# Kernel optimization log

Hardware: AMD Instinct MI355X
Metric: run time of the kernel (lower is better)

Reference implementation:

```python
import jax, jax.numpy as jnp
import numpy as np

D = 1024      # d_model
H = 8         # heads
DH = D // H
L = 12        # layers
E = 4         # experts
F = 2048      # dim_feedforward
NCLS = 10
SPARSITY = 0.5
EPS = 1e-5
B, S = 4, 512


def _xavier(key, shape):
    fan_in, fan_out = shape[-1], shape[-2] if len(shape) > 1 else shape[-1]
    scale = jnp.sqrt(2.0 / (fan_in + fan_out))
    return jax.random.normal(key, shape, jnp.float32) * scale


def setup_inputs() -> dict:
    key = jax.random.key(0)
    ks = jax.random.split(key, 16)
    return {
        "x": jax.random.normal(ks[0], (B, S, D), jnp.float32),
        "pos": jax.random.normal(ks[1], (1, 512, D), jnp.float32) * 0.02,
        # stacked per-layer transformer params
        "Wqkv": _xavier(ks[2], (L, 3 * D, D)), "bqkv": jnp.zeros((L, 3 * D), jnp.float32),
        "Wo": _xavier(ks[3], (L, D, D)),       "bo": jnp.zeros((L, D), jnp.float32),
        "ln1_s": jnp.ones((L, D), jnp.float32), "ln1_b": jnp.zeros((L, D), jnp.float32),
        "W1": _xavier(ks[4], (L, F, D)), "b1": jnp.zeros((L, F), jnp.float32),
        "W2": _xavier(ks[5], (L, D, F)), "b2": jnp.zeros((L, D), jnp.float32),
        "ln2_s": jnp.ones((L, D), jnp.float32), "ln2_b": jnp.zeros((L, D), jnp.float32),
        # shared gate / experts / classifier
        "Wg": _xavier(ks[6], (E, D)), "bg": jnp.zeros((E,), jnp.float32),
        "We": _xavier(ks[7], (E, D, D)), "be": jnp.zeros((E, D), jnp.float32),
        "Wf": _xavier(ks[8], (NCLS, D)), "bf": jnp.zeros((NCLS,), jnp.float32),
    }


def _layernorm(x, s, b):
    m = jnp.mean(x, axis=-1, keepdims=True)
    v = jnp.mean(jnp.square(x - m), axis=-1, keepdims=True)
    return (x - m) * jax.lax.rsqrt(v + EPS) * s + b


def _forward(x, pos, Wqkv, bqkv, Wo, bo, ln1_s, ln1_b, W1, b1, W2, b2,
             ln2_s, ln2_b, Wg, bg, We, be, Wf, bf):
    Bx, Sx, _ = x.shape
    x = x + pos[:, :Sx, :]
    for l in range(L):
        # --- self-attention (post-norm TransformerEncoderLayer, eval/no-dropout) ---
        qkv = x @ Wqkv[l].T + bqkv[l]                      # [B,S,3D]
        q, k, v = jnp.split(qkv, 3, axis=-1)
        q = q.reshape(Bx, Sx, H, DH).transpose(0, 2, 1, 3)  # bhsd
        k = k.reshape(Bx, Sx, H, DH).transpose(0, 2, 1, 3)
        v = v.reshape(Bx, Sx, H, DH).transpose(0, 2, 1, 3)
        attn = jax.nn.softmax(jnp.einsum('bhqd,bhkd->bhqk', q, k) / jnp.sqrt(jnp.float32(DH)), axis=-1)
        o = jnp.einsum('bhqk,bhkd->bhqd', attn, v).transpose(0, 2, 1, 3).reshape(Bx, Sx, D)
        o = o @ Wo[l].T + bo[l]
        x = _layernorm(x + o, ln1_s[l], ln1_b[l])
        # --- ffn (exact gelu) ---
        h = jax.nn.gelu(x @ W1[l].T + b1[l], approximate=False) @ W2[l].T + b2[l]
        x = _layernorm(x + h, ln2_s[l], ln2_b[l])
        # --- top-2 gated MoE (shared gate/experts across layers) ---
        gs = jax.nn.softmax(x @ Wg.T + bg, axis=-1)         # [B,S,E]
        vals, idx = jax.lax.top_k(gs, 2)                    # [B,S,2]
        all_out = jnp.einsum('bsd,eod->bseo', x, We) + be   # [B,S,E,D]
        sel = jnp.take_along_axis(all_out, idx[..., None], axis=2)  # [B,S,2,D]
        expert_out = jnp.sum(sel * vals[..., None], axis=2)
        x = x * (1.0 - SPARSITY) + expert_out * SPARSITY
    return x[:, -1, :] @ Wf.T + bf                          # [B,10]


def reference(x, pos, Wqkv, bqkv, Wo, bo, ln1_s, ln1_b, W1, b1, W2, b2,
              ln2_s, ln2_b, Wg, bg, We, be, Wf, bf):
    return _forward(x, pos, Wqkv, bqkv, Wo, bo, ln1_s, ln1_b, W1, b1, W2, b2,
                    ln2_s, ln2_b, Wg, bg, We, be, Wf, bf)
```

## Files before the change

### kernel.cpp

```cpp
#include <hip/hip_runtime.h>
#include <math.h>

#define D     1024
#define NH    8
#define DHD   128
#define NL    12
#define NE    4
#define FF    2048
#define NCLS  10
#define BB    4
#define SS    512
#define TT    (BB*SS)
#define EPSV  1e-5f
#define SPARS 0.5f

typedef __attribute__((ext_vector_type(8))) short bf16x8;
typedef __attribute__((ext_vector_type(4))) float f32x4;
typedef unsigned short ushortT;

__device__ __forceinline__ ushortT f2bf(float f) {
    unsigned u = __float_as_uint(f);
    u += 0x7FFF + ((u >> 16) & 1);
    return (ushortT)(u >> 16);
}
__device__ __forceinline__ float bf2f(ushortT h) {
    return __uint_as_float(((unsigned)h) << 16);
}

__global__ __launch_bounds__(256)
void wconv(const float* __restrict__ in, ushortT* __restrict__ out, long n)
{
    const long stride = (long)gridDim.x * 256 * 8;
    for (long i = ((long)blockIdx.x * 256 + threadIdx.x) * 8; i < n; i += stride) {
        float f[8];
        *reinterpret_cast<float4*>(f)   = *reinterpret_cast<const float4*>(in + i);
        *reinterpret_cast<float4*>(f+4) = *reinterpret_cast<const float4*>(in + i + 4);
        bf16x8 u;
        #pragma unroll
        for (int e = 0; e < 8; ++e) ((ushortT*)&u)[e] = f2bf(f[e]);
        *reinterpret_cast<bf16x8*>(out + i) = u;
    }
}

#define LDP 40

template<int MODE, int SK, int ACT, int BN>
__global__ __launch_bounds__(256)
void gemm_mfma(const ushortT* __restrict__ A, const ushortT* __restrict__ Bw,
               const float* __restrict__ bias, void* __restrict__ Cv,
               int M, int N, int Ktot, int Klen, long eBw, long eBias, long eC)
{
    const int z = blockIdx.z;
    int koff = 0;
    float* Cf = nullptr; ushortT* Ch = nullptr;
    if constexpr (SK > 1) {
        koff = z * Klen;
        Cf = (float*)Cv + (size_t)z * M * N;
    } else {
        Bw   += (size_t)z * eBw;
        bias += (size_t)z * eBias;
        if constexpr (MODE == 0) Ch = (ushortT*)Cv + (size_t)z * eC;
        else                     Cf = (float*)Cv   + (size_t)z * eC;
    }

    constexpr int MR = (BN == 128) ? 4 : 2;
    __shared__ ushortT Asl[128 * LDP];
    __shared__ ushortT Bsl[BN * LDP];

    const int tid  = threadIdx.x;
    const int wave = tid >> 6, lane = tid & 63;
    const int wm = (BN == 128) ? (wave >> 1) * 64 : wave * 32;
    const int wn = (BN == 128) ? (wave & 1) * 64 : 0;
    const int fr = lane & 15;
    const int fq = lane >> 4;

    const int m0 = blockIdx.y * 128;
    const int n0 = blockIdx.x * BN;

    const int arow = tid >> 1;
    const int akc  = (tid & 1) * 16;
    const ushortT* Ag = A + (size_t)(m0 + arow) * Ktot + koff + akc;
    const int brow = (BN == 128) ? (tid >> 1) : (tid >> 2);
    const int bkc  = (BN == 128) ? (tid & 1) * 16 : (tid & 3) * 8;
    const ushortT* Bg = Bw + (size_t)(n0 + brow) * Ktot + koff + bkc;

    f32x4 acc[MR][4] = {};

    for (int k0 = 0; k0 < Klen; k0 += 32) {
        bf16x8 av8[2], bv8[2];
        av8[0] = *reinterpret_cast<const bf16x8*>(Ag + k0);
        av8[1] = *reinterpret_cast<const bf16x8*>(Ag + k0 + 8);
        bv8[0] = *reinterpret_cast<const bf16x8*>(Bg + k0);
        if constexpr (BN == 128)
            bv8[1] = *reinterpret_cast<const bf16x8*>(Bg + k0 + 8);
        __syncthreads();
        *reinterpret_cast<bf16x8*>(&Asl[arow*LDP + akc])     = av8[0];
        *reinterpret_cast<bf16x8*>(&Asl[arow*LDP + akc + 8]) = av8[1];
        *reinterpret_cast<bf16x8*>(&Bsl[brow*LDP + bkc])     = bv8[0];
        if constexpr (BN == 128)
            *reinterpret_cast<bf16x8*>(&Bsl[brow*LDP + bkc + 8]) = bv8[1];
        __syncthreads();

        bf16x8 af[MR], bfr[4];
        #pragma unroll
        for (int i = 0; i < MR; ++i)
            af[i]  = *reinterpret_cast<const bf16x8*>(&Asl[(wm + i*16 + fr)*LDP + fq*8]);
        #pragma unroll
        for (int j = 0; j < 4; ++j)
            bfr[j] = *reinterpret_cast<const bf16x8*>(&Bsl[(wn + j*16 + fr)*LDP + fq*8]);
        #pragma unroll
        for (int i = 0; i < MR; ++i)
            #pragma unroll
            for (int j = 0; j < 4; ++j)
                acc[i][j] = __builtin_amdgcn_mfma_f32_16x16x32_bf16(af[i], bfr[j], acc[i][j], 0, 0, 0);
    }

    #pragma unroll
    for (int j = 0; j < 4; ++j) {
        const int n = n0 + wn + j*16 + fr;
        float bb = 0.f;
        if constexpr (SK == 1) bb = bias[n];
        #pragma unroll
        for (int i = 0; i < MR; ++i) {
            const int mb = m0 + wm + i*16 + fq*4;
            if constexpr (SK > 1) {
                #pragma unroll
                for (int r = 0; r < 4; ++r)
                    Cf[(size_t)(mb + r) * N + n] = acc[i][j][r];
            } else if constexpr (MODE == 0) {
                #pragma unroll
                for (int r = 0; r < 4; ++r) {
                    float u = acc[i][j][r] + bb;
                    if constexpr (ACT == 1) u = 0.5f*u*(1.0f + erff(u*0.70710678118654752f));
                    Ch[(size_t)(mb + r) * N + n] = f2bf(u);
                }
            } else {
                #pragma unroll
                for (int r = 0; r < 4; ++r) {
                    float u = acc[i][j][r] + bb;
                    if constexpr (ACT == 1) u = 0.5f*u*(1.0f + erff(u*0.70710678118654752f));
                    Cf[(size_t)(mb + r) * N + n] = u;
                }
            }
        }
    }
}

__global__ __launch_bounds__(256)
void kv_prep(const float* __restrict__ qkv, ushortT* __restrict__ Kb, ushortT* __restrict__ Vt)
{
    __shared__ ushortT T[64*136];
    const int tid = threadIdx.x;
    const int st = blockIdx.x, bh = blockIdx.y;
    const int b = bh >> 3, h = bh & 7;
    const float* base = qkv + (size_t)(b*SS + st*64)*3*D + h*DHD;

    #pragma unroll
    for (int p = 0; p < 4; ++p) {
        const int row = (tid >> 4) + 16*p;
        const int colb = (tid & 15) * 8;
        {
            const float* src = base + (size_t)row*3*D + D + colb;
            float f[8];
            *reinterpret_cast<float4*>(f)   = *reinterpret_cast<const float4*>(src);
            *reinterpret_cast<float4*>(f+4) = *reinterpret_cast<const float4*>(src+4);
            bf16x8 u;
            #pragma unroll
            for (int e = 0; e < 8; ++e) ((ushortT*)&u)[e] = f2bf(f[e]);
            *reinterpret_cast<bf16x8*>(&Kb[((size_t)bh*SS + st*64 + row)*DHD + colb]) = u;
        }
        {
            const float* src = base + (size_t)row*3*D + 2*D + colb;
            float f[8];
            *reinterpret_cast<float4*>(f)   = *reinterpret_cast<const float4*>(src);
            *reinterpret_cast<float4*>(f+4) = *reinterpret_cast<const float4*>(src+4);
            #pragma unroll
            for (int e = 0; e < 8; ++e) T[row*136 + colb + e] = f2bf(f[e]);
        }
    }
    __syncthreads();
    #pragma unroll
    for (int p = 0; p < 4; ++p) {
        const int d  = (tid >> 3) + 32*p;
        const int sb = (tid & 7) * 8;
        bf16x8 u;
        #pragma unroll
        for (int e = 0; e < 8; ++e) ((ushortT*)&u)[e] = T[(sb + e)*136 + d];
        *reinterpret_cast<bf16x8*>(&Vt[((size_t)bh*DHD + d)*SS + st*64 + sb]) = u;
    }
}

#define KLP 136
#define VLP 72
#define PLP 72

__global__ __launch_bounds__(256)
void attn_mfma(const float* __restrict__ qkv, const ushortT* __restrict__ Kb,
               const ushortT* __restrict__ Vt, ushortT* __restrict__ o16)
{
    __shared__ ushortT Kl[64*KLP];
    __shared__ ushortT Vl[128*VLP];
    __shared__ ushortT Pl[4*16*PLP];

    const int tid = threadIdx.x;
    const int w = tid >> 6, lane = tid & 63;
    const int g = lane >> 4, c = lane & 15;
    const int bh = blockIdx.y;
    const int b = bh >> 3, h = bh & 7;
    const int q0 = blockIdx.x*64 + w*16;
    ushortT* Pw = Pl + w*16*PLP;

    bf16x8 qhi[4], qlo[4];
    const float scale = 0.08838834764831845f;
    {
        const float* Qrow = qkv + (size_t)(b*SS + q0 + c)*3*D + h*DHD;
        #pragma unroll
        for (int db = 0; db < 4; ++db) {
            float f[8];
            *reinterpret_cast<float4*>(f)   = *reinterpret_cast<const float4*>(Qrow + db*32 + g*8);
            *reinterpret_cast<float4*>(f+4) = *reinterpret_cast<const float4*>(Qrow + db*32 + g*8 + 4);
            #pragma unroll
            for (int e = 0; e < 8; ++e) {
                const float fs = f[e]*scale;
                const ushortT hi = f2bf(fs);
                ((ushortT*)&qhi[db])[e] = hi;
                ((ushortT*)&qlo[db])[e] = f2bf(fs - bf2f(hi));
            }
        }
    }

    const ushortT* Kg = Kb + (size_t)bh*SS*DHD;
    const ushortT* Vg = Vt + (size_t)bh*DHD*SS;

    float m_r[4], l_r[4];
    #pragma unroll
    for (int r = 0; r < 4; ++r) { m_r[r] = -1e30f; l_r[r] = 0.f; }
    f32x4 oacc[8] = {};

    for (int kt = 0; kt < SS/64; ++kt) {
        __syncthreads();
        #pragma unroll
        for (int p = 0; p < 4; ++p) {
            const int row = (tid >> 4) + 16*p;
            const int colb = (tid & 15)*8;
            bf16x8 u = *reinterpret_cast<const bf16x8*>(&Kg[(size_t)(kt*64 + row)*DHD + colb]);
            *reinterpret_cast<bf16x8*>(&Kl[row*KLP + colb]) = u;
        }
        #pragma unroll
        for (int p = 0; p < 4; ++p) {
            const int dr = (tid >> 3) + 32*p;
            const int sb = (tid & 7)*8;
            bf16x8 u = *reinterpret_cast<const bf16x8*>(&Vg[(size_t)dr*SS + kt*64 + sb]);
            *reinterpret_cast<bf16x8*>(&Vl[dr*VLP + sb]) = u;
        }
        __syncthreads();

        f32x4 s[4] = {};
        #pragma unroll
        for (int db = 0; db < 4; ++db) {
            bf16x8 kf[4];
            #pragma unroll
            for (int kb = 0; kb < 4; ++kb)
                kf[kb] = *reinterpret_cast<const bf16x8*>(&Kl[(kb*16 + c)*KLP + db*32 + g*8]);
            #pragma unroll
            for (int kb = 0; kb < 4; ++kb) {
                s[kb] = __builtin_amdgcn_mfma_f32_16x16x32_bf16(qhi[db], kf[kb], s[kb], 0, 0, 0);
                s[kb] = __builtin_amdgcn_mfma_f32_16x16x32_bf16(qlo[db], kf[kb], s[kb], 0, 0, 0);
            }
        }

        float tmax[4];
        #pragma unroll
        for (int r = 0; r < 4; ++r)
            tmax[r] = fmaxf(fmaxf(s[0][r], s[1][r]), fmaxf(s[2][r], s[3][r]));
        #pragma unroll
        for (int off = 1; off < 16; off <<= 1)
            #pragma unroll
            for (int r = 0; r < 4; ++r)
                tmax[r] = fmaxf(tmax[r], __shfl_xor(tmax[r], off));
        float mn[4], corr[4];
        #pragma unroll
        for (int r = 0; r < 4; ++r) {
            mn[r] = fmaxf(m_r[r], tmax[r]);
            corr[r] = __expf(m_r[r] - mn[r]);
            m_r[r] = mn[r];
        }
        float tsum[4] = {0.f, 0.f, 0.f, 0.f};
        #pragma unroll
        for (int kb = 0; kb < 4; ++kb)
            #pragma unroll
            for (int r = 0; r < 4; ++r) {
                const float p = __expf(s[kb][r] - mn[r]);
                s[kb][r] = p;
                tsum[r] += p;
            }
        #pragma unroll
        for (int off = 1; off < 16; off <<= 1)
            #pragma unroll
            for (int r = 0; r < 4; ++r)
                tsum[r] += __shfl_xor(tsum[r], off);
        #pragma unroll
        for (int r = 0; r < 4; ++r) l_r[r] = l_r[r]*corr[r] + tsum[r];
        #pragma unroll
        for (int df = 0; df < 8; ++df)
            #pragma unroll
            for (int r = 0; r < 4; ++r)
                oacc[df][r] *= corr[r];

        #pragma unroll
        for (int kb = 0; kb < 4; ++kb)
            #pragma unroll
            for (int r = 0; r < 4; ++r)
                Pw[(g*4 + r)*PLP + kb*16 + c] = f2bf(s[kb][r]);

        #pragma unroll
        for (int kk = 0; kk < 2; ++kk) {
            bf16x8 pa = *reinterpret_cast<const bf16x8*>(&Pw[c*PLP + kk*32 + g*8]);
            #pragma unroll
            for (int df = 0; df < 8; ++df) {
                bf16x8 vb = *reinterpret_cast<const bf16x8*>(&Vl[(df*16 + c)*VLP + kk*32 + g*8]);
                oacc[df] = __builtin_amdgcn_mfma_f32_16x16x32_bf16(pa, vb, oacc[df], 0, 0, 0);
            }
        }
    }

    #pragma unroll
    for (int r = 0; r < 4; ++r) {
        const float inv = 1.0f / l_r[r];
        ushortT* orow = o16 + (size_t)(b*SS + q0 + g*4 + r)*D + h*DHD + c;
        #pragma unroll
        for (int df = 0; df < 8; ++df)
            orow[df*16] = f2bf(oacc[df][r] * inv);
    }
}

template<int SK, int GATE>
__global__ __launch_bounds__(256)
void add_ln_r(const float* __restrict__ xin, const float* __restrict__ P,
              const float* __restrict__ dbias,
              const float* __restrict__ gs, const float* __restrict__ gb,
              float* __restrict__ x32, ushortT* __restrict__ x16,
              const float* __restrict__ Wg, const float* __restrict__ bg,
              float* __restrict__ gv, int* __restrict__ gi)
{
    const int row = blockIdx.x, tid = threadIdx.x;
    const size_t off = (size_t)row*D + tid*4;
    float4 a = *reinterpret_cast<const float4*>(xin + off);
    float d0, d1, d2, d3;
    {
        float4 bvd = *reinterpret_cast<const float4*>(dbias + tid*4);
        d0 = bvd.x; d1 = bvd.y; d2 = bvd.z; d3 = bvd.w;
    }
    #pragma unroll
    for (int s = 0; s < SK; ++s) {
        float4 pv = *reinterpret_cast<const float4*>(P + (size_t)s*TT*D + off);
        d0 += pv.x; d1 += pv.y; d2 += pv.z; d3 += pv.w;
    }
    float v0=a.x+d0, v1=a.y+d1, v2=a.z+d2, v3=a.w+d3;
    __shared__ float red[2][4];
    float s = v0+v1+v2+v3;
    #pragma unroll
    for (int o = 32; o; o >>= 1) s += __shfl_xor(s, o, 64);
    if ((tid & 63) == 0) red[0][tid>>6] = s;
    __syncthreads();
    const float mean = (red[0][0]+red[0][1]+red[0][2]+red[0][3]) * (1.0f/D);
    v0-=mean; v1-=mean; v2-=mean; v3-=mean;
    float qv = v0*v0+v1*v1+v2*v2+v3*v3;
    #pragma unroll
    for (int o = 32; o; o >>= 1) qv += __shfl_xor(qv, o, 64);
    if ((tid & 63) == 0) red[1][tid>>6] = qv;
    __syncthreads();
    const float var = (red[1][0]+red[1][1]+red[1][2]+red[1][3]) * (1.0f/D);
    const float rstd = rsqrtf(var + EPSV);
    float4 sv = *reinterpret_cast<const float4*>(gs + tid*4);
    float4 bv = *reinterpret_cast<const float4*>(gb + tid*4);
    float ov[4];
    ov[0] = v0*rstd*sv.x + bv.x;
    ov[1] = v1*rstd*sv.y + bv.y;
    ov[2] = v2*rstd*sv.z + bv.z;
    ov[3] = v3*rstd*sv.w + bv.w;
    float4 o4; o4.x=ov[0]; o4.y=ov[1]; o4.z=ov[2]; o4.w=ov[3];
    *reinterpret_cast<float4*>(x32 + off) = o4;
    ushort4 h4; h4.x=f2bf(ov[0]); h4.y=f2bf(ov[1]); h4.z=f2bf(ov[2]); h4.w=f2bf(ov[3]);
    *reinterpret_cast<ushort4*>(x16 + off) = h4;

    if constexpr (GATE) {
        float p[4] = {0.f, 0.f, 0.f, 0.f};
        #pragma unroll
        for (int e = 0; e < 4; ++e) {
            const float* wr = Wg + (size_t)e*D + tid*4;
            p[e] = ov[0]*wr[0] + ov[1]*wr[1] + ov[2]*wr[2] + ov[3]*wr[3];
        }
        #pragma unroll
        for (int o = 32; o; o >>= 1) {
            p[0] += __shfl_xor(p[0], o, 64); p[1] += __shfl_xor(p[1], o, 64);
            p[2] += __shfl_xor(p[2], o, 64); p[3] += __shfl_xor(p[3], o, 64);
        }
        __shared__ float gred[4][4];
        if ((tid & 63) == 0) {
            const int w = tid>>6;
            gred[w][0]=p[0]; gred[w][1]=p[1]; gred[w][2]=p[2]; gred[w][3]=p[3];
        }
        __syncthreads();
        if (tid == 0) {
            float g[4];
            #pragma unroll
            for (int e = 0; e < 4; ++e) g[e] = gred[0][e]+gred[1][e]+gred[2][e]+gred[3][e] + bg[e];
            const float mx = fmaxf(fmaxf(g[0],g[1]), fmaxf(g[2],g[3]));
            float ssum = 0.f;
            #pragma unroll
            for (int e = 0; e < 4; ++e) { g[e] = __expf(g[e]-mx); ssum += g[e]; }
            const float inv = 1.0f/ssum;
            #pragma unroll
            for (int e = 0; e < 4; ++e) g[e] *= inv;
            int i0 = 0;
            for (int e = 1; e < 4; ++e) if (g[e] > g[i0]) i0 = e;
            int i1 = (i0 == 0) ? 1 : 0;
            for (int e = 0; e < 4; ++e) if (e != i0 && g[e] > g[i1]) i1 = e;
            gv[row*2]   = g[i0]; gv[row*2+1] = g[i1];
            gi[row*2]   = i0;    gi[row*2+1] = i1;
        }
    }
}

__global__ __launch_bounds__(256)
void moe_combine(float* __restrict__ x, ushortT* __restrict__ x16,
                 const float* __restrict__ eo,
                 const float* __restrict__ gv, const int* __restrict__ gi)
{
    const size_t i = (size_t)blockIdx.x*256 + threadIdx.x;
    const int t = (int)(i >> 10);
    const float w0 = gv[t*2]*SPARS, w1 = gv[t*2+1]*SPARS;
    const size_t TD = (size_t)TT*D;
    const float e0 = eo[(size_t)gi[t*2]*TD + i];
    const float e1 = eo[(size_t)gi[t*2+1]*TD + i];
    const float r = x[i]*(1.0f-SPARS) + w0*e0 + w1*e1;
    x[i] = r;
    x16[i] = f2bf(r);
}

__global__ __launch_bounds__(256)
void addpos(const float* __restrict__ xin, const float* __restrict__ pos,
            float* __restrict__ xo, ushortT* __restrict__ x16)
{
    const size_t i = (size_t)blockIdx.x*256 + threadIdx.x;
    const float r = xin[i] + pos[i & ((size_t)SS*D - 1)];
    xo[i] = r;
    x16[i] = f2bf(r);
}

__global__ __launch_bounds__(64)
void final_kernel(const float* __restrict__ x, const float* __restrict__ Wf,
                  const float* __restrict__ bf, float* __restrict__ out)
{
    const int b = blockIdx.x / NCLS, n = blockIdx.x % NCLS;
    const float* xr = x + ((size_t)b*SS + SS-1)*D;
    const int tid = threadIdx.x;
    float s = 0.f;
    for (int d = tid; d < D; d += 64) s += xr[d]*Wf[(size_t)n*D + d];
    #pragma unroll
    for (int o = 32; o; o >>= 1) s += __shfl_xor(s, o, 64);
    if (tid == 0) out[b*NCLS + n] = s + bf[n];
}

extern "C" void kernel_launch(void* const* d_in, const int* in_sizes, int n_in,
                              void* d_out, int out_size, void* d_ws, size_t ws_size,
                              hipStream_t stream)
{
    const float* x_in = (const float*)d_in[0];
    const float* pos  = (const float*)d_in[1];
    const float* Wqkv = (const float*)d_in[2];
    const float* bqkv = (const float*)d_in[3];
    const float* Wo   = (const float*)d_in[4];
    const float* bo   = (const float*)d_in[5];
    const float* ln1s = (const float*)d_in[6];
    const float* ln1b = (const float*)d_in[7];
    const float* W1   = (const float*)d_in[8];
    const float* b1   = (const float*)d_in[9];
    const float* W2   = (const float*)d_in[10];
    const float* b2   = (const float*)d_in[11];
    const float* ln2s = (const float*)d_in[12];
    const float* ln2b = (const float*)d_in[13];
    const float* Wg   = (const float*)d_in[14];
    const float* bg   = (const float*)d_in[15];
    const float* We   = (const float*)d_in[16];
    const float* be   = (const float*)d_in[17];
    const float* Wf   = (const float*)d_in[18];
    const float* bf   = (const float*)d_in[19];
    float* out = (float*)d_out;

    const long nWqkv = (long)NL*3*D*D;
    const long nWo   = (long)NL*D*D;
    const long nW1   = (long)NL*FF*D;
    const long nW2   = (long)NL*D*FF;
    const long nWe   = (long)NE*D*D;

    float* ws     = (float*)d_ws;
    float*   xbuf  = ws;
    ushortT* xb16  = (ushortT*)(xbuf + (size_t)TT*D);
    ushortT* ob16  = xb16 + (size_t)TT*D;
    float*   scratch = (float*)(ob16 + (size_t)TT*D);
    ushortT* hb16 = (ushortT*)(scratch + (size_t)TT*D*4);
    float*   gv    = (float*)(hb16 + (size_t)TT*FF);
    int*     gi    = (int*)(gv + (size_t)TT*2);
    ushortT* wq16  = (ushortT*)(gi + (size_t)TT*2);
    ushortT* wo16  = wq16 + nWqkv;
    ushortT* w116  = wo16 + nWo;
    ushortT* w216  = w116 + nW1;
    ushortT* we16  = w216 + nW2;
    float*   qkvbuf = scratch;
    ushortT* Kb     = (ushortT*)(qkvbuf + (size_t)TT*3*D);
    ushortT* Vt     = Kb + (size_t)BB*NH*SS*DHD;
    float*   parts  = scratch;
    float*   ebuf   = scratch;

    const dim3 blk(256);
    wconv<<<dim3(2048), blk, 0, stream>>>(Wqkv, wq16, nWqkv);
    wconv<<<dim3(1024), blk, 0, stream>>>(Wo,   wo16, nWo);
    wconv<<<dim3(2048), blk, 0, stream>>>(W1,   w116, nW1);
    wconv<<<dim3(2048), blk, 0, stream>>>(W2,   w216, nW2);
    wconv<<<dim3(512),  blk, 0, stream>>>(We,   we16, nWe);

    addpos<<<dim3(TT*D/256), blk, 0, stream>>>(x_in, pos, xbuf, xb16);

    for (int l = 0; l < NL; ++l) {
        gemm_mfma<1,1,0,64><<<dim3(3*D/64, TT/128, 1), blk, 0, stream>>>(
            xb16, wq16 + (size_t)l*3*D*D, bqkv + (size_t)l*3*D, qkvbuf,
            TT, 3*D, D, D, 0, 0, 0);
        kv_prep<<<dim3(SS/64, BB*NH), blk, 0, stream>>>(qkvbuf, Kb, Vt);
        attn_mfma<<<dim3(SS/64, BB*NH), blk, 0, stream>>>(qkvbuf, Kb, Vt, ob16);
        gemm_mfma<1,4,0,128><<<dim3(D/128, TT/128, 4), blk, 0, stream>>>(
            ob16, wo16 + (size_t)l*D*D, bo, parts, TT, D, D, D/4, 0, 0, 0);
        add_ln_r<4,0><<<dim3(TT), blk, 0, stream>>>(
            xbuf, parts, bo + (size_t)l*D, ln1s + (size_t)l*D, ln1b + (size_t)l*D,
            xbuf, xb16, nullptr, nullptr, nullptr, nullptr);
        gemm_mfma<0,1,1,64><<<dim3(FF/64, TT/128, 1), blk, 0, stream>>>(
            xb16, w116 + (size_t)l*FF*D, b1 + (size_t)l*FF, hb16, TT, FF, D, D, 0, 0, 0);
        gemm_mfma<1,4,0,128><<<dim3(D/128, TT/128, 4), blk, 0, stream>>>(
            hb16, w216 + (size_t)l*D*FF, b2, parts, TT, D, FF, FF/4, 0, 0, 0);
        add_ln_r<4,1><<<dim3(TT), blk, 0, stream>>>(
            xbuf, parts, b2 + (size_t)l*D, ln2s + (size_t)l*D, ln2b + (size_t)l*D,
            xbuf, xb16, Wg, bg, gv, gi);
        gemm_mfma<1,1,0,64><<<dim3(D/64, TT/128, NE), blk, 0, stream>>>(
            xb16, we16, be, ebuf, TT, D, D, D, (long)D*D, (long)D, (long)TT*D);
        moe_combine<<<dim3(TT*D/256), blk, 0, stream>>>(xbuf, xb16, ebuf, gv, gi);
    }
    final_kernel<<<dim3(BB*NCLS), dim3(64), 0, stream>>>(xbuf, Wf, bf, out);
}
```

Measured before the change: 2.591 ms.

## Fuse QKV split/convert into GEMM epilogue and prefetch next K tile

The QKV GEMM epilogue now writes Q as fp32 in a compact layout, K directly as bf16 in head-major layout, and V as bf16, so the old kv_prep pass only has to transpose bf16 V. This removes the full fp32 qkv round trip for K and V. Separately, the GEMM main loop now loads the next K-slice from global memory into registers before the MFMA work on the current slice, overlapping load latency with compute at the cost of extra registers. The epilogue stores for K are scattered at 2-byte granularity, which may reduce write efficiency.

```diff
diff --git a/kernel.cpp b/kernel.cpp
--- a/kernel.cpp
+++ b/kernel.cpp
@@ -44,11 +44,12 @@
 
 #define LDP 40
 
-template<int MODE, int SK, int ACT, int BN>
+template<int MODE, int SK, int ACT, int BN, int EPI>
 __global__ __launch_bounds__(256)
 void gemm_mfma(const ushortT* __restrict__ A, const ushortT* __restrict__ Bw,
                const float* __restrict__ bias, void* __restrict__ Cv,
-               int M, int N, int Ktot, int Klen, long eBw, long eBias, long eC)
+               int M, int N, int Ktot, int Klen, long eBw, long eBias, long eC,
+               float* __restrict__ qp, ushortT* __restrict__ kp, ushortT* __restrict__ vp)
 {
     const int z = blockIdx.z;
     int koff = 0;
@@ -85,14 +86,15 @@
     const ushortT* Bg = Bw + (size_t)(n0 + brow) * Ktot + koff + bkc;
 
     f32x4 acc[MR][4] = {};
+    bf16x8 av8[2], bv8[2];
+
+    av8[0] = *reinterpret_cast<const bf16x8*>(Ag);
+    av8[1] = *reinterpret_cast<const bf16x8*>(Ag + 8);
+    bv8[0] = *reinterpret_cast<const bf16x8*>(Bg);
+    if constexpr (BN == 128)
+        bv8[1] = *reinterpret_cast<const bf16x8*>(Bg + 8);
 
     for (int k0 = 0; k0 < Klen; k0 += 32) {
-        bf16x8 av8[2], bv8[2];
-        av8[0] = *reinterpret_cast<const bf16x8*>(Ag + k0);
-        av8[1] = *reinterpret_cast<const bf16x8*>(Ag + k0 + 8);
-        bv8[0] = *reinterpret_cast<const bf16x8*>(Bg + k0);
-        if constexpr (BN == 128)
-            bv8[1] = *reinterpret_cast<const bf16x8*>(Bg + k0 + 8);
         __syncthreads();
         *reinterpret_cast<bf16x8*>(&Asl[arow*LDP + akc])     = av8[0];
         *reinterpret_cast<bf16x8*>(&Asl[arow*LDP + akc + 8]) = av8[1];
@@ -101,6 +103,15 @@
             *reinterpret_cast<bf16x8*>(&Bsl[brow*LDP + bkc + 8]) = bv8[1];
         __syncthreads();
 
+        const int kn = k0 + 32;
+        if (kn < Klen) {
+            av8[0] = *reinterpret_cast<const bf16x8*>(Ag + kn);
+            av8[1] = *reinterpret_cast<const bf16x8*>(Ag + kn + 8);
+            bv8[0] = *reinterpret_cast<const bf16x8*>(Bg + kn);
+            if constexpr (BN == 128)
+                bv8[1] = *reinterpret_cast<const bf16x8*>(Bg + kn + 8);
+        }
+
         bf16x8 af[MR], bfr[4];
         #pragma unroll
         for (int i = 0; i < MR; ++i)
@@ -123,7 +134,23 @@
         #pragma unroll
         for (int i = 0; i < MR; ++i) {
             const int mb = m0 + wm + i*16 + fq*4;
-            if constexpr (SK > 1) {
+            if constexpr (EPI == 1) {
+                #pragma unroll
+                for (int r = 0; r < 4; ++r) {
+                    const float u = acc[i][j][r] + bb;
+                    const int t = mb + r;
+                    if (n0 < D) {
+                        qp[(size_t)t*D + n] = u;
+                    } else if (n0 < 2*D) {
+                        const int n2 = n - D;
+                        const int hh = n2 >> 7, dd = n2 & 127;
+                        const int bb_ = t >> 9, ss_ = t & 511;
+                        kp[(((size_t)bb_*NH + hh)*SS + ss_)*DHD + dd] = f2bf(u);
+                    } else {
+                        vp[(size_t)t*D + (n - 2*D)] = f2bf(u);
+                    }
+                }
+            } else if constexpr (SK > 1) {
                 #pragma unroll
                 for (int r = 0; r < 4; ++r)
                     Cf[(size_t)(mb + r) * N + n] = acc[i][j][r];
@@ -147,36 +174,20 @@
 }
 
 __global__ __launch_bounds__(256)
-void kv_prep(const float* __restrict__ qkv, ushortT* __restrict__ Kb, ushortT* __restrict__ Vt)
+void v_tr(const ushortT* __restrict__ Vb, ushortT* __restrict__ Vt)
 {
     __shared__ ushortT T[64*136];
     const int tid = threadIdx.x;
     const int st = blockIdx.x, bh = blockIdx.y;
     const int b = bh >> 3, h = bh & 7;
-    const float* base = qkv + (size_t)(b*SS + st*64)*3*D + h*DHD;
+    const ushortT* base = Vb + (size_t)(b*SS + st*64)*D + h*DHD;
 
     #pragma unroll
     for (int p = 0; p < 4; ++p) {
         const int row = (tid >> 4) + 16*p;
         const int colb = (tid & 15) * 8;
-        {
-            const float* src = base + (size_t)row*3*D + D + colb;
-            float f[8];
-            *reinterpret_cast<float4*>(f)   = *reinterpret_cast<const float4*>(src);
-            *reinterpret_cast<float4*>(f+4) = *reinterpret_cast<const float4*>(src+4);
-            bf16x8 u;
-            #pragma unroll
-            for (int e = 0; e < 8; ++e) ((ushortT*)&u)[e] = f2bf(f[e]);
-            *reinterpret_cast<bf16x8*>(&Kb[((size_t)bh*SS + st*64 + row)*DHD + colb]) = u;
-        }
-        {
-            const float* src = base + (size_t)row*3*D + 2*D + colb;
-            float f[8];
-            *reinterpret_cast<float4*>(f)   = *reinterpret_cast<const float4*>(src);
-            *reinterpret_cast<float4*>(f+4) = *reinterpret_cast<const float4*>(src+4);
-            #pragma unroll
-            for (int e = 0; e < 8; ++e) T[row*136 + colb + e] = f2bf(f[e]);
-        }
+        bf16x8 u = *reinterpret_cast<const bf16x8*>(base + (size_t)row*D + colb);
+        *reinterpret_cast<bf16x8*>(&T[row*136 + colb]) = u;
     }
     __syncthreads();
     #pragma unroll
@@ -195,7 +206,7 @@
 #define PLP 72
 
 __global__ __launch_bounds__(256)
-void attn_mfma(const float* __restrict__ qkv, const ushortT* __restrict__ Kb,
+void attn_mfma(const float* __restrict__ Qb, const ushortT* __restrict__ Kb,
                const ushortT* __restrict__ Vt, ushortT* __restrict__ o16)
 {
     __shared__ ushortT Kl[64*KLP];
@@ -213,7 +224,7 @@
     bf16x8 qhi[4], qlo[4];
     const float scale = 0.08838834764831845f;
     {
-        const float* Qrow = qkv + (size_t)(b*SS + q0 + c)*3*D + h*DHD;
+        const float* Qrow = Qb + (size_t)(b*SS + q0 + c)*D + h*DHD;
         #pragma unroll
         for (int db = 0; db < 4; ++db) {
             float f[8];
@@ -508,9 +519,10 @@
     ushortT* w116  = wo16 + nWo;
     ushortT* w216  = w116 + nW1;
     ushortT* we16  = w216 + nW2;
-    float*   qkvbuf = scratch;
-    ushortT* Kb     = (ushortT*)(qkvbuf + (size_t)TT*3*D);
-    ushortT* Vt     = Kb + (size_t)BB*NH*SS*DHD;
+    float*   Qbuf = scratch;
+    ushortT* Kb   = (ushortT*)(Qbuf + (size_t)TT*D);
+    ushortT* Vb   = Kb + (size_t)TT*D;
+    ushortT* Vt   = Vb + (size_t)TT*D;
     float*   parts  = scratch;
     float*   ebuf   = scratch;
 
@@ -524,25 +536,29 @@
     addpos<<<dim3(TT*D/256), blk, 0, stream>>>(x_in, pos, xbuf, xb16);
 
     for (int l = 0; l < NL; ++l) {
-        gemm_mfma<1,1,0,64><<<dim3(3*D/64, TT/128, 1), blk, 0, stream>>>(
-            xb16, wq16 + (size_t)l*3*D*D, bqkv + (size_t)l*3*D, qkvbuf,
-            TT, 3*D, D, D, 0, 0, 0);
-        kv_prep<<<dim3(SS/64, BB*NH), blk, 0, stream>>>(qkvbuf, Kb, Vt);
-        attn_mfma<<<dim3(SS/64, BB*NH), blk, 0, stream>>>(qkvbuf, Kb, Vt, ob16);
-        gemm_mfma<1,4,0,128><<<dim3(D/128, TT/128, 4), blk, 0, stream>>>(
-            ob16, wo16 + (size_t)l*D*D, bo, parts, TT, D, D, D/4, 0, 0, 0);
+        gemm_mfma<1,1,0,64,1><<<dim3(3*D/64, TT/128, 1), blk, 0, stream>>>(
+            xb16, wq16 + (size_t)l*3*D*D, bqkv + (size_t)l*3*D, nullptr,
+            TT, 3*D, D, D, 0, 0, 0, Qbuf, Kb, Vb);
+        v_tr<<<dim3(SS/64, BB*NH), blk, 0, stream>>>(Vb, Vt);
+        attn_mfma<<<dim3(SS/64, BB*NH), blk, 0, stream>>>(Qbuf, Kb, Vt, ob16);
+        gemm_mfma<1,4,0,128,0><<<dim3(D/128, TT/128, 4), blk, 0, stream>>>(
+            ob16, wo16 + (size_t)l*D*D, bo, parts, TT, D, D, D/4, 0, 0, 0,
+            nullptr, nullptr, nullptr);
         add_ln_r<4,0><<<dim3(TT), blk, 0, stream>>>(
             xbuf, parts, bo + (size_t)l*D, ln1s + (size_t)l*D, ln1b + (size_t)l*D,
             xbuf, xb16, nullptr, nullptr, nullptr, nullptr);
-        gemm_mfma<0,1,1,64><<<dim3(FF/64, TT/128, 1), blk, 0, stream>>>(
-            xb16, w116 + (size_t)l*FF*D, b1 + (size_t)l*FF, hb16, TT, FF, D, D, 0, 0, 0);
-        gemm_mfma<1,4,0,128><<<dim3(D/128, TT/128, 4), blk, 0, stream>>>(
-            hb16, w216 + (size_t)l*D*FF, b2, parts, TT, D, FF, FF/4, 0, 0, 0);
+        gemm_mfma<0,1,1,64,0><<<dim3(FF/64, TT/128, 1), blk, 0, stream>>>(
+            xb16, w116 + (size_t)l*FF*D, b1 + (size_t)l*FF, hb16, TT, FF, D, D, 0, 0, 0,
+            nullptr, nullptr, nullptr);
+        gemm_mfma<1,4,0,128,0><<<dim3(D/128, TT/128, 4), blk, 0, stream>>>(
+            hb16, w216 + (size_t)l*D*FF, b2, parts, TT, D, FF, FF/4, 0, 0, 0,
+            nullptr, nullptr, nullptr);
         add_ln_r<4,1><<<dim3(TT), blk, 0, stream>>>(
             xbuf, parts, b2 + (size_t)l*D, ln2s + (size_t)l*D, ln2b + (size_t)l*D,
             xbuf, xb16, Wg, bg, gv, gi);
-        gemm_mfma<1,1,0,64><<<dim3(D/64, TT/128, NE), blk, 0, stream>>>(
-            xb16, we16, be, ebuf, TT, D, D, D, (long)D*D, (long)D, (long)TT*D);
+        gemm_mfma<1,1,0,64,0><<<dim3(D/64, TT/128, NE), blk, 0, stream>>>(
+            xb16, we16, be, ebuf, TT, D, D, D, (long)D*D, (long)D, (long)TT*D,
+            nullptr, nullptr, nullptr);
         moe_combine<<<dim3(TT*D/256), blk, 0, stream>>>(xbuf, xb16, ebuf, gv, gi);
     }
     final_kernel<<<dim3(BB*NCLS), dim3(64), 0, stream>>>(xbuf, Wf, bf, out);
```

Result: faster. 2.422 ms (-6.5%).
